# Kernel tuning notes

Measured on AMD Instinct MI355X. Metric: run time of the kernel, lower is better.

Reference implementation:

```python
import jax, jax.numpy as jnp
import numpy as np


def setup_inputs() -> dict:
    key = jax.random.key(0)
    ks = jax.random.split(key, 5)
    B, C, H, W = 4, 256, 64, 64
    Cq = C // 8
    x = jax.random.normal(ks[0], (B, C, H, W), dtype=jnp.float32)
    Wq = jax.random.normal(ks[1], (Cq, C), dtype=jnp.float32) * (1.0 / np.sqrt(C))
    Wk = jax.random.normal(ks[2], (Cq, C), dtype=jnp.float32) * (1.0 / np.sqrt(C))
    Wv = jax.random.normal(ks[3], (C, C), dtype=jnp.float32) * (1.0 / np.sqrt(C))
    bq = jnp.zeros((Cq,), dtype=jnp.float32)
    bk = jnp.zeros((Cq,), dtype=jnp.float32)
    bv = jnp.zeros((C,), dtype=jnp.float32)
    gamma = jnp.ones((1,), dtype=jnp.float32)
    return {"x": x, "Wq": Wq, "bq": bq, "Wk": Wk, "bk": bk, "Wv": Wv, "bv": bv, "gamma": gamma}


def reference(x, Wq, bq, Wk, bk, Wv, bv, gamma):
    B, C, H, W = x.shape
    N = H * W
    xf = x.reshape(B, C, N)                      # (B, C, N)
    # 1x1 convs == per-pixel linear projections over channels
    q = jnp.einsum('dc,bcn->bdn', Wq, xf) + bq[None, :, None]   # (B, C/8, N)
    k = jnp.einsum('dc,bcn->bdn', Wk, xf) + bk[None, :, None]   # (B, C/8, N)
    v = jnp.einsum('dc,bcn->bdn', Wv, xf) + bv[None, :, None]   # (B, C,   N)
    # attention: note original has NO 1/sqrt(d) scaling
    scores = jnp.einsum('bdn,bdm->bnm', q, k)     # (B, N, N)
    attn = jax.nn.softmax(scores, axis=-1)
    out = jnp.einsum('bnm,bdm->bnd', attn, v)     # (B, N, C)
    out = out.transpose(0, 2, 1).reshape(B, C, H, W)
    return gamma * out + x
```

## Files before the change

kernel.cpp:

```cpp
#include <hip/hip_runtime.h>

#define BATCH 4
#define CH    256
#define DQ    32
#define NPIX  4096
#define LOG2E 1.44269504088896340736f

typedef unsigned short u16;
typedef unsigned int   u32;
typedef __attribute__((ext_vector_type(8))) short short8;
typedef __attribute__((ext_vector_type(16))) float f32x16;

__device__ __align__(16) u16 g_wbf[10 * 2 * 8192];
__device__ float g_bias[10 * 32];

__device__ __forceinline__ float b2f(u32 u) {
  union { u32 i; float f; } v; v.i = (u & 0xffffu) << 16; return v.f;
}
__device__ __forceinline__ u16 f2b(float f) {
  union { float f; u32 i; } v; v.f = f;
  u32 x = v.i; x += 0x7fffu + ((x >> 16) & 1u);
  return (u16)(x >> 16);
}
__device__ __forceinline__ float fexp2(float x) {
#if __has_builtin(__builtin_amdgcn_exp2f)
  return __builtin_amdgcn_exp2f(x);
#else
  return __expf(x * 0.69314718055994530942f);
#endif
}

__device__ __forceinline__ void half_swap(u32 a0, u32 a1, u32 b0, u32 b1,
                                          int hl, uint4& o) {
#if __has_builtin(__builtin_amdgcn_permlane32_swap)
  const auto r0 = __builtin_amdgcn_permlane32_swap((int)a0, (int)b0, false, false);
  const auto r1 = __builtin_amdgcn_permlane32_swap((int)a1, (int)b1, false, false);
  o.x = (u32)r0[0]; o.y = (u32)r1[0]; o.z = (u32)r0[1]; o.w = (u32)r1[1];
#else
  const u32 s0 = hl ? a0 : b0;
  const u32 s1 = hl ? a1 : b1;
  const u32 r0 = (u32)__shfl_xor((int)s0, 32);
  const u32 r1 = (u32)__shfl_xor((int)s1, 32);
  o.x = hl ? r0 : a0; o.y = hl ? r1 : a1;
  o.z = hl ? b0 : r0; o.w = hl ? b1 : r1;
#endif
}

__global__ __launch_bounds__(256) void xprep(
    const float* __restrict__ x, u16* __restrict__ xt_hi, u16* __restrict__ xt_lo,
    const float* __restrict__ Wq, const float* __restrict__ bq,
    const float* __restrict__ Wk, const float* __restrict__ bk,
    const float* __restrict__ Wv, const float* __restrict__ bv)
{
  const int t = threadIdx.x;

  if (blockIdx.z == BATCH) {
    if (blockIdx.y != 0 || blockIdx.x >= 10) return;
    const int jt = blockIdx.x;
    const float* Wsrc; const float* bsrc; int jrow0; float scale = 1.f;
    if (jt == 0)      { Wsrc = Wq; bsrc = bq; jrow0 = 0; scale = LOG2E; }
    else if (jt == 1) { Wsrc = Wk; bsrc = bk; jrow0 = 0; }
    else              { Wsrc = Wv; bsrc = bv; jrow0 = (jt - 2) * 32; }
    u16* wdst = g_wbf + (size_t)jt * 16384;
    for (int i = 0; i < 32; ++i) {
      const int flat = i * 256 + t;
      const int j = flat >> 8, e = flat & 255;
      const float v = Wsrc[(size_t)(jrow0 + j) * CH + e] * scale;
      const u16 hi = f2b(v);
      const u16 lo = f2b(v - b2f(hi));
      const int idx = (((e >> 4) * 2 + ((e >> 3) & 1)) * 32 + j) * 8 + (e & 7);
      wdst[idx] = hi; wdst[8192 + idx] = lo;
    }
    if (t < 32) g_bias[jt * 32 + t] = bsrc[jrow0 + t] * scale;
    return;
  }

  const int nt = blockIdx.x, kb4 = blockIdx.y * 4, b = blockIdx.z;
  const int n0 = nt * 128, c0 = blockIdx.y * 64;
  __shared__ u32 xls[64][129];

  const int tn = t & 127, cp = t >> 7;
  for (int i = 0; i < 32; ++i) {
    const int c = cp + 2 * i;
    const float v = x[((size_t)b * CH + c0 + c) * NPIX + n0 + tn];
    const u16 h = f2b(v);
    const u16 l = f2b(v - b2f(h));
    xls[c][tn] = (u32)h | ((u32)l << 16);
  }
  __syncthreads();

  for (int rep = 0; rep < 4; ++rep) {
    const int id = t + 256 * rep;
    const int kkhl = id >> 7, n = id & 127;
    union { short8 s; uint4 u; } vh, vl;
    #pragma unroll
    for (int j = 0; j < 8; ++j) {
      const u32 p = xls[kkhl * 8 + j][n];
      vh.s[j] = (short)(p & 0xffffu);
      vl.s[j] = (short)(p >> 16);
    }
    const size_t o = ((((size_t)(b * 32 + nt) * 16 + kb4 + (kkhl >> 1)) * 2
                       + (kkhl & 1)) * 128 + n) * 8;
    *(uint4*)(xt_hi + o) = vh.u;
    *(uint4*)(xt_lo + o) = vl.u;
  }
}

__global__ __launch_bounds__(256, 4) void proj(
    const u16* __restrict__ xt_hi, const u16* __restrict__ xt_lo,
    u16* __restrict__ q_t, u16* __restrict__ k_t, u16* __restrict__ v_swz)
{
  const int L = blockIdx.x;
  const int xcd = L & 7, s = L >> 3;
  const int jt = s >> 4;
  const int pair = xcd * 16 + (s & 15);
  const int nt = pair >> 2, b = pair & 3;

  const int t = threadIdx.x;
  const int w = t >> 6, lane = t & 63, hl = lane >> 5, l31 = lane & 31;
  const int nb = w * 32 + l31, n = nt * 128 + nb;

  const u16* __restrict__ wb = g_wbf + (size_t)jt * 16384;
  const size_t xtile = (size_t)(b * 32 + nt) * 16 * 2 * 128 * 8;
  const u16* __restrict__ xh = xt_hi + xtile;
  const u16* __restrict__ xl = xt_lo + xtile;

  f32x16 acc1, acc2;
  #pragma unroll
  for (int r = 0; r < 16; ++r) { acc1[r] = 0.f; acc2[r] = 0.f; }

  #pragma unroll
  for (int kk = 0; kk < 16; ++kk) {
    const int aoff = ((kk * 2 + hl) * 32 + l31) * 8;
    const short8 wah = *(const short8*)(wb + aoff);
    const short8 wal = *(const short8*)(wb + 8192 + aoff);
    const int boff = ((kk * 2 + hl) * 128 + nb) * 8;
    const short8 xbh = *(const short8*)(xh + boff);
    const short8 xbl = *(const short8*)(xl + boff);
    acc1 = __builtin_amdgcn_mfma_f32_32x32x16_bf16(wah, xbh, acc1, 0, 0, 0);
    acc2 = __builtin_amdgcn_mfma_f32_32x32x16_bf16(wah, xbl, acc2, 0, 0, 0);
    acc2 = __builtin_amdgcn_mfma_f32_32x32x16_bf16(wal, xbh, acc2, 0, 0, 0);
  }

  f32x16 accv;
  #pragma unroll
  for (int r = 0; r < 16; ++r)
    accv[r] = acc1[r] + acc2[r]
            + g_bias[jt * 32 + (r & 3) + 8 * (r >> 2) + 4 * hl];

  if (jt <= 1) {
    u16* dst = (jt == 0) ? q_t : k_t;
    #pragma unroll
    for (int r2 = 0; r2 < 4; ++r2) {
      uint2 pk;
      pk.x = (u32)f2b(accv[4 * r2 + 0]) | ((u32)f2b(accv[4 * r2 + 1]) << 16);
      pk.y = (u32)f2b(accv[4 * r2 + 2]) | ((u32)f2b(accv[4 * r2 + 3]) << 16);
      *(uint2*)(dst + ((size_t)b * NPIX + n) * DQ + 4 * hl + 8 * r2) = pk;
    }
  } else {
    const int mc = nt * 4 + w;
    const int kc = (l31 >> 4) & 1, h3 = (l31 >> 3) & 1, j8 = l31 & 7;
    u16* dst = v_swz + (((((size_t)b * 128 + mc) * 8 + (jt - 2)) * 2 + kc) * 2 + h3) * 256 + j8;
    #pragma unroll
    for (int r = 0; r < 16; ++r) {
      const int c5 = (r & 3) + 8 * (r >> 2) + 4 * hl;
      dst[c5 * 8] = f2b(accv[r]);
    }
  }
}

__global__ __launch_bounds__(256, 2) void attn(
    const u16* __restrict__ q_t, const u16* __restrict__ k_t,
    const u16* __restrict__ v_swz, const float* __restrict__ x,
    const float* __restrict__ gamma, float* __restrict__ out)
{
  const int L = blockIdx.x;
  const int xcd = L & 7, slot = L >> 3;
  const int b = xcd >> 1;
  const int nt = slot * 2 + (xcd & 1);
  const int n0 = nt * 32;

  const int t = threadIdx.x;
  const int w = t >> 6, lane = t & 63, hl = lane >> 5, l31 = lane & 31;

  __shared__ float cbuf[8192];
  __shared__ float lbuf[4][64];

  short8 qf[2];
  #pragma unroll
  for (int kd = 0; kd < 2; ++kd)
    qf[kd] = *(const short8*)(q_t + ((size_t)b * NPIX + n0 + l31) * DQ + kd * 16 + hl * 8);

  f32x16 acc[8];
  #pragma unroll
  for (int ct = 0; ct < 8; ++ct)
    #pragma unroll
    for (int r = 0; r < 16; ++r) acc[ct][r] = 0.f;
  float lrun = 0.f;

  for (int cc = 0; cc < 32; ++cc) {
    const int mc = w * 32 + cc;

    const short8 kf0 = *(const short8*)(k_t + ((size_t)b * NPIX + mc * 32 + l31) * DQ + hl * 8);
    const short8 kf1 = *(const short8*)(k_t + ((size_t)b * NPIX + mc * 32 + l31) * DQ + 16 + hl * 8);
    f32x16 st;
    #pragma unroll
    for (int r = 0; r < 16; ++r) st[r] = 0.f;
    st = __builtin_amdgcn_mfma_f32_32x32x16_bf16(kf0, qf[0], st, 0, 0, 0);
    st = __builtin_amdgcn_mfma_f32_32x32x16_bf16(kf1, qf[1], st, 0, 0, 0);

    u32 pk[4][2];
    #pragma unroll
    for (int g = 0; g < 4; ++g) {
      const float e0 = fexp2(st[4 * g + 0]);
      const float e1 = fexp2(st[4 * g + 1]);
      const float e2 = fexp2(st[4 * g + 2]);
      const float e3 = fexp2(st[4 * g + 3]);
      lrun += (e0 + e1) + (e2 + e3);
      pk[g][0] = (u32)f2b(e0) | ((u32)f2b(e1) << 16);
      pk[g][1] = (u32)f2b(e2) | ((u32)f2b(e3) << 16);
    }

    const size_t vbase = ((size_t)b * 128 + mc) * 8192;
    #pragma unroll
    for (int kc = 0; kc < 2; ++kc) {
      union { uint4 u; short8 s; } bu;
      half_swap(pk[2 * kc][0], pk[2 * kc][1], pk[2 * kc + 1][0], pk[2 * kc + 1][1], hl, bu.u);
      #pragma unroll
      for (int ct = 0; ct < 8; ++ct) {
        const short8 av = *(const short8*)(v_swz + vbase + (size_t)(((ct * 2 + kc) * 2 + hl) * 256) + l31 * 8);
        acc[ct] = __builtin_amdgcn_mfma_f32_32x32x16_bf16(av, bu.s, acc[ct], 0, 0, 0);
      }
    }
  }

  lbuf[w][lane] = lrun;
  __syncthreads();
  for (int src = 1; src < 4; ++src) {
    if (w == src) {
      #pragma unroll
      for (int ct = 0; ct < 8; ++ct)
        #pragma unroll
        for (int r = 0; r < 16; ++r)
          cbuf[(ct * 16 + r) * 64 + lane] = acc[ct][r];
    }
    __syncthreads();
    if (w == 0) {
      #pragma unroll
      for (int ct = 0; ct < 8; ++ct)
        #pragma unroll
        for (int r = 0; r < 16; ++r)
          acc[ct][r] += cbuf[(ct * 16 + r) * 64 + lane];
    }
    __syncthreads();
  }

  if (w == 0) {
    float l = (lbuf[0][lane] + lbuf[1][lane]) + (lbuf[2][lane] + lbuf[3][lane]);
    l += __shfl_xor(l, 32);
    const float linv = 1.0f / l;
    const float g = gamma[0];
    #pragma unroll
    for (int ct = 0; ct < 8; ++ct)
      #pragma unroll
      for (int r = 0; r < 16; ++r) {
        const int c = ct * 32 + (r & 3) + 8 * (r >> 2) + 4 * hl;
        const size_t idx = ((size_t)b * CH + c) * NPIX + n0 + l31;
        out[idx] = g * acc[ct][r] * linv + x[idx];
      }
  }
}

extern "C" void kernel_launch(void* const* d_in, const int* in_sizes, int n_in,
                              void* d_out, int out_size, void* d_ws, size_t ws_size,
                              hipStream_t stream) {
  const float* x  = (const float*)d_in[0];
  const float* Wq = (const float*)d_in[1];
  const float* bq = (const float*)d_in[2];
  const float* Wk = (const float*)d_in[3];
  const float* bk = (const float*)d_in[4];
  const float* Wv = (const float*)d_in[5];
  const float* bv = (const float*)d_in[6];
  const float* gm = (const float*)d_in[7];
  float* out = (float*)d_out;

  const size_t qk_elems = (size_t)BATCH * NPIX * DQ;
  const size_t v_elems  = (size_t)BATCH * NPIX * CH;
  const size_t need = (2 * qk_elems + v_elems) * sizeof(u16);
  if (ws_size < need) return;

  u16* q_t   = (u16*)d_ws;
  u16* k_t   = q_t + qk_elems;
  u16* v_swz = k_t + qk_elems;

  u16* xt_hi = (u16*)d_out;
  u16* xt_lo = xt_hi + (size_t)BATCH * NPIX * CH;

  xprep<<<dim3(NPIX / 128, CH / 64, BATCH + 1), 256, 0, stream>>>(
      x, xt_hi, xt_lo, Wq, bq, Wk, bk, Wv, bv);
  proj<<<dim3(32 * 10 * BATCH), 256, 0, stream>>>(xt_hi, xt_lo, q_t, k_t, v_swz);
  attn<<<dim3((NPIX / 32) * BATCH), 256, 0, stream>>>(q_t, k_t, v_swz, x, gm, out);
}
```

Measured before the change: 160.3 us.

## Widen attention tile to 64 queries with 8 warps splitting keys and channels

The attention kernel now processes 64 query columns per block using 512 threads. Warps are split into 4 key groups by 2 channel halves, so each V fragment load feeds two MFMAs (one per 32-query subtile), halving V traffic per output. The cross-warp reduction now accumulates in shared memory with all threads doing a coalesced epilogue rather than warp 0 alone, and bf16 packing uses the hardware v_cvt_pk_bf16_f32 instruction. In exchange, shared memory doubles to 64KB plus accumulators per thread, which may cut occupancy, and the grid shrinks to 256 blocks.

```diff
diff --git a/kernel.cpp b/kernel.cpp
--- a/kernel.cpp
+++ b/kernel.cpp
@@ -28,6 +28,11 @@
 #else
   return __expf(x * 0.69314718055994530942f);
 #endif
+}
+__device__ __forceinline__ u32 cvtpk_bf16(float a, float b) {
+  u32 r;
+  asm("v_cvt_pk_bf16_f32 %0, %1, %2" : "=v"(r) : "v"(a), "v"(b));
+  return r;
 }
 
 __device__ __forceinline__ void half_swap(u32 a0, u32 a1, u32 b0, u32 b1,
@@ -169,7 +174,7 @@
   }
 }
 
-__global__ __launch_bounds__(256, 2) void attn(
+__global__ __launch_bounds__(512, 2) void attn(
     const u16* __restrict__ q_t, const u16* __restrict__ k_t,
     const u16* __restrict__ v_swz, const float* __restrict__ x,
     const float* __restrict__ gamma, float* __restrict__ out)
@@ -177,97 +182,115 @@
   const int L = blockIdx.x;
   const int xcd = L & 7, slot = L >> 3;
   const int b = xcd >> 1;
-  const int nt = slot * 2 + (xcd & 1);
-  const int n0 = nt * 32;
+  const int ng = slot * 2 + (xcd & 1);
+  const int n0 = ng * 64;
 
   const int t = threadIdx.x;
   const int w = t >> 6, lane = t & 63, hl = lane >> 5, l31 = lane & 31;
-
-  __shared__ float cbuf[8192];
-  __shared__ float lbuf[4][64];
-
-  short8 qf[2];
-  #pragma unroll
-  for (int kd = 0; kd < 2; ++kd)
-    qf[kd] = *(const short8*)(q_t + ((size_t)b * NPIX + n0 + l31) * DQ + kd * 16 + hl * 8);
-
-  f32x16 acc[8];
-  #pragma unroll
-  for (int ct = 0; ct < 8; ++ct)
-    #pragma unroll
-    for (int r = 0; r < 16; ++r) acc[ct][r] = 0.f;
-  float lrun = 0.f;
+  const int g = w >> 1, h = w & 1;
+
+  __shared__ float cbuf[16384];
+  __shared__ float lbuf[4][2][64];
+
+  short8 qf[2][2];
+  #pragma unroll
+  for (int jn = 0; jn < 2; ++jn)
+    #pragma unroll
+    for (int kd = 0; kd < 2; ++kd)
+      qf[jn][kd] = *(const short8*)(q_t + ((size_t)b * NPIX + n0 + jn * 32 + l31) * DQ + kd * 16 + hl * 8);
+
+  f32x16 acc[4][2];
+  #pragma unroll
+  for (int c = 0; c < 4; ++c)
+    #pragma unroll
+    for (int jn = 0; jn < 2; ++jn)
+      #pragma unroll
+      for (int r = 0; r < 16; ++r) acc[c][jn][r] = 0.f;
+  float lr[2] = {0.f, 0.f};
+
+  const u16* __restrict__ kb = k_t + (size_t)b * NPIX * DQ;
+  const u16* __restrict__ vb = v_swz + ((size_t)b * 128) * 8192
+                               + h * 4096 + hl * 256 + l31 * 8;
 
   for (int cc = 0; cc < 32; ++cc) {
-    const int mc = w * 32 + cc;
-
-    const short8 kf0 = *(const short8*)(k_t + ((size_t)b * NPIX + mc * 32 + l31) * DQ + hl * 8);
-    const short8 kf1 = *(const short8*)(k_t + ((size_t)b * NPIX + mc * 32 + l31) * DQ + 16 + hl * 8);
-    f32x16 st;
-    #pragma unroll
-    for (int r = 0; r < 16; ++r) st[r] = 0.f;
-    st = __builtin_amdgcn_mfma_f32_32x32x16_bf16(kf0, qf[0], st, 0, 0, 0);
-    st = __builtin_amdgcn_mfma_f32_32x32x16_bf16(kf1, qf[1], st, 0, 0, 0);
-
-    u32 pk[4][2];
-    #pragma unroll
-    for (int g = 0; g < 4; ++g) {
-      const float e0 = fexp2(st[4 * g + 0]);
-      const float e1 = fexp2(st[4 * g + 1]);
-      const float e2 = fexp2(st[4 * g + 2]);
-      const float e3 = fexp2(st[4 * g + 3]);
-      lrun += (e0 + e1) + (e2 + e3);
-      pk[g][0] = (u32)f2b(e0) | ((u32)f2b(e1) << 16);
-      pk[g][1] = (u32)f2b(e2) | ((u32)f2b(e3) << 16);
-    }
-
-    const size_t vbase = ((size_t)b * 128 + mc) * 8192;
-    #pragma unroll
-    for (int kc = 0; kc < 2; ++kc) {
-      union { uint4 u; short8 s; } bu;
-      half_swap(pk[2 * kc][0], pk[2 * kc][1], pk[2 * kc + 1][0], pk[2 * kc + 1][1], hl, bu.u);
-      #pragma unroll
-      for (int ct = 0; ct < 8; ++ct) {
-        const short8 av = *(const short8*)(v_swz + vbase + (size_t)(((ct * 2 + kc) * 2 + hl) * 256) + l31 * 8);
-        acc[ct] = __builtin_amdgcn_mfma_f32_32x32x16_bf16(av, bu.s, acc[ct], 0, 0, 0);
+    const int mc = g * 32 + cc;
+
+    const short8 kf0 = *(const short8*)(kb + (mc * 32 + l31) * DQ + hl * 8);
+    const short8 kf1 = *(const short8*)(kb + (mc * 32 + l31) * DQ + 16 + hl * 8);
+
+    u32 pk[2][4][2];
+    #pragma unroll
+    for (int jn = 0; jn < 2; ++jn) {
+      f32x16 st;
+      #pragma unroll
+      for (int r = 0; r < 16; ++r) st[r] = 0.f;
+      st = __builtin_amdgcn_mfma_f32_32x32x16_bf16(kf0, qf[jn][0], st, 0, 0, 0);
+      st = __builtin_amdgcn_mfma_f32_32x32x16_bf16(kf1, qf[jn][1], st, 0, 0, 0);
+      #pragma unroll
+      for (int g4 = 0; g4 < 4; ++g4) {
+        const float e0 = fexp2(st[4 * g4 + 0]);
+        const float e1 = fexp2(st[4 * g4 + 1]);
+        const float e2 = fexp2(st[4 * g4 + 2]);
+        const float e3 = fexp2(st[4 * g4 + 3]);
+        lr[jn] += (e0 + e1) + (e2 + e3);
+        pk[jn][g4][0] = cvtpk_bf16(e0, e1);
+        pk[jn][g4][1] = cvtpk_bf16(e2, e3);
       }
     }
-  }
-
-  lbuf[w][lane] = lrun;
+
+    union { uint4 u; short8 s; } bu[2][2];
+    #pragma unroll
+    for (int jn = 0; jn < 2; ++jn)
+      #pragma unroll
+      for (int kc = 0; kc < 2; ++kc)
+        half_swap(pk[jn][2 * kc][0], pk[jn][2 * kc][1],
+                  pk[jn][2 * kc + 1][0], pk[jn][2 * kc + 1][1], hl, bu[jn][kc].u);
+
+    const u16* __restrict__ vpt = vb + (size_t)mc * 8192;
+    #pragma unroll
+    for (int c = 0; c < 4; ++c)
+      #pragma unroll
+      for (int kc = 0; kc < 2; ++kc) {
+        const short8 av = *(const short8*)(vpt + c * 1024 + kc * 512);
+        acc[c][0] = __builtin_amdgcn_mfma_f32_32x32x16_bf16(av, bu[0][kc].s, acc[c][0], 0, 0, 0);
+        acc[c][1] = __builtin_amdgcn_mfma_f32_32x32x16_bf16(av, bu[1][kc].s, acc[c][1], 0, 0, 0);
+      }
+  }
+
+  if (h == 0) { lbuf[g][0][lane] = lr[0]; lbuf[g][1][lane] = lr[1]; }
+
+  for (int gs = 0; gs < 4; ++gs) {
+    __syncthreads();
+    if (g == gs) {
+      #pragma unroll
+      for (int c = 0; c < 4; ++c)
+        #pragma unroll
+        for (int jn = 0; jn < 2; ++jn)
+          #pragma unroll
+          for (int r = 0; r < 16; ++r) {
+            const int ch = (h * 4 + c) * 32 + (r & 3) + 8 * (r >> 2) + 4 * hl;
+            const int idx = (jn * 256 + ch) * 32 + l31;
+            if (gs == 0) cbuf[idx] = acc[c][jn][r];
+            else         cbuf[idx] += acc[c][jn][r];
+          }
+    }
+  }
   __syncthreads();
-  for (int src = 1; src < 4; ++src) {
-    if (w == src) {
-      #pragma unroll
-      for (int ct = 0; ct < 8; ++ct)
-        #pragma unroll
-        for (int r = 0; r < 16; ++r)
-          cbuf[(ct * 16 + r) * 64 + lane] = acc[ct][r];
-    }
-    __syncthreads();
-    if (w == 0) {
-      #pragma unroll
-      for (int ct = 0; ct < 8; ++ct)
-        #pragma unroll
-        for (int r = 0; r < 16; ++r)
-          acc[ct][r] += cbuf[(ct * 16 + r) * 64 + lane];
-    }
-    __syncthreads();
-  }
-
-  if (w == 0) {
-    float l = (lbuf[0][lane] + lbuf[1][lane]) + (lbuf[2][lane] + lbuf[3][lane]);
-    l += __shfl_xor(l, 32);
-    const float linv = 1.0f / l;
-    const float g = gamma[0];
-    #pragma unroll
-    for (int ct = 0; ct < 8; ++ct)
-      #pragma unroll
-      for (int r = 0; r < 16; ++r) {
-        const int c = ct * 32 + (r & 3) + 8 * (r >> 2) + 4 * hl;
-        const size_t idx = ((size_t)b * CH + c) * NPIX + n0 + l31;
-        out[idx] = g * acc[ct][r] * linv + x[idx];
-      }
+
+  const int col = t & 63, chg = t >> 6;
+  const int jn = col >> 5, c31 = col & 31;
+  float l = 0.f;
+  #pragma unroll
+  for (int gg = 0; gg < 4; ++gg)
+    l += lbuf[gg][jn][c31] + lbuf[gg][jn][c31 + 32];
+  const float linv = 1.0f / l;
+  const float gmv = gamma[0];
+  #pragma unroll
+  for (int i = 0; i < 32; ++i) {
+    const int ch = chg * 32 + i;
+    const float cb = cbuf[(jn * 256 + ch) * 32 + c31];
+    const size_t oidx = ((size_t)b * CH + ch) * NPIX + n0 + col;
+    out[oidx] = gmv * cb * linv + x[oidx];
   }
 }
 
@@ -299,5 +322,5 @@
   xprep<<<dim3(NPIX / 128, CH / 64, BATCH + 1), 256, 0, stream>>>(
       x, xt_hi, xt_lo, Wq, bq, Wk, bk, Wv, bv);
   proj<<<dim3(32 * 10 * BATCH), 256, 0, stream>>>(xt_hi, xt_lo, q_t, k_t, v_swz);
-  attn<<<dim3((NPIX / 32) * BATCH), 256, 0, stream>>>(q_t, k_t, v_swz, x, gm, out);
-}
+  attn<<<dim3((NPIX / 64) * BATCH), 512, 0, stream>>>(q_t, k_t, v_swz, x, gm, out);
+}
```

Result: slower. 173.7 us (+8.3%).

## Double-buffer V fragments in registers and software-pipeline QK scores in attention loop

Applied to the files above, without the earlier changes.

Restructures the attention main loop into a two-stage software pipeline. V tiles for the next key chunk are loaded into a second register buffer while the current chunk's exp and PV MFMAs run, and the next QK score MFMA is issued before the PV products. It also replaces the manual bf16 rounding with the packed v_cvt_pk_bf16_f32 instruction and relaxes launch bounds to one block per SM so the larger register footprint fits. This trades occupancy for latency hiding through explicit prefetch.

```diff
diff --git a/kernel.cpp b/kernel.cpp
--- a/kernel.cpp
+++ b/kernel.cpp
@@ -28,6 +28,11 @@
 #else
   return __expf(x * 0.69314718055994530942f);
 #endif
+}
+__device__ __forceinline__ u32 cvtpk_bf16(float a, float b) {
+  u32 r;
+  asm("v_cvt_pk_bf16_f32 %0, %1, %2" : "=v"(r) : "v"(a), "v"(b));
+  return r;
 }
 
 __device__ __forceinline__ void half_swap(u32 a0, u32 a1, u32 b0, u32 b1,
@@ -169,7 +174,7 @@
   }
 }
 
-__global__ __launch_bounds__(256, 2) void attn(
+__global__ __launch_bounds__(256, 1) void attn(
     const u16* __restrict__ q_t, const u16* __restrict__ k_t,
     const u16* __restrict__ v_swz, const float* __restrict__ x,
     const float* __restrict__ gamma, float* __restrict__ out)
@@ -198,18 +203,41 @@
     for (int r = 0; r < 16; ++r) acc[ct][r] = 0.f;
   float lrun = 0.f;
 
-  for (int cc = 0; cc < 32; ++cc) {
-    const int mc = w * 32 + cc;
-
-    const short8 kf0 = *(const short8*)(k_t + ((size_t)b * NPIX + mc * 32 + l31) * DQ + hl * 8);
-    const short8 kf1 = *(const short8*)(k_t + ((size_t)b * NPIX + mc * 32 + l31) * DQ + 16 + hl * 8);
-    f32x16 st;
-    #pragma unroll
-    for (int r = 0; r < 16; ++r) st[r] = 0.f;
-    st = __builtin_amdgcn_mfma_f32_32x32x16_bf16(kf0, qf[0], st, 0, 0, 0);
-    st = __builtin_amdgcn_mfma_f32_32x32x16_bf16(kf1, qf[1], st, 0, 0, 0);
-
-    u32 pk[4][2];
+  const u16* __restrict__ kb = k_t + (size_t)b * NPIX * DQ;
+  const u16* __restrict__ vp = v_swz + ((size_t)b * 128) * 8192
+                               + hl * 256 + l31 * 8;
+
+  short8 va[16], vb[16];
+
+  auto vload = [&](short8* A, int mcx) {
+    const u16* vt = vp + (size_t)mcx * 8192;
+    #pragma unroll
+    for (int kc = 0; kc < 2; ++kc)
+      #pragma unroll
+      for (int ct = 0; ct < 8; ++ct)
+        A[kc * 8 + ct] = *(const short8*)(vt + (ct * 2 + kc) * 512);
+  };
+  auto sstep = [&](int mcx) {
+    const short8 kf0 = *(const short8*)(kb + (mcx * 32 + l31) * DQ + hl * 8);
+    const short8 kf1 = *(const short8*)(kb + (mcx * 32 + l31) * DQ + 16 + hl * 8);
+    f32x16 s;
+    #pragma unroll
+    for (int r = 0; r < 16; ++r) s[r] = 0.f;
+    s = __builtin_amdgcn_mfma_f32_32x32x16_bf16(kf0, qf[0], s, 0, 0, 0);
+    s = __builtin_amdgcn_mfma_f32_32x32x16_bf16(kf1, qf[1], s, 0, 0, 0);
+    return s;
+  };
+
+  vload(va, w * 32);
+  f32x16 st = sstep(w * 32);
+
+  for (int cc2 = 0; cc2 < 16; ++cc2) {
+    const int mcA = w * 32 + 2 * cc2;
+    const int mcB = mcA + 1;
+    const int mcN = (2 * cc2 + 1 < 31) ? mcB + 1 : mcB;
+
+    vload(vb, mcB);
+    u32 pkA[4][2];
     #pragma unroll
     for (int g = 0; g < 4; ++g) {
       const float e0 = fexp2(st[4 * g + 0]);
@@ -217,20 +245,39 @@
       const float e2 = fexp2(st[4 * g + 2]);
       const float e3 = fexp2(st[4 * g + 3]);
       lrun += (e0 + e1) + (e2 + e3);
-      pk[g][0] = (u32)f2b(e0) | ((u32)f2b(e1) << 16);
-      pk[g][1] = (u32)f2b(e2) | ((u32)f2b(e3) << 16);
-    }
-
-    const size_t vbase = ((size_t)b * 128 + mc) * 8192;
+      pkA[g][0] = cvtpk_bf16(e0, e1);
+      pkA[g][1] = cvtpk_bf16(e2, e3);
+    }
+    st = sstep(mcB);
     #pragma unroll
     for (int kc = 0; kc < 2; ++kc) {
       union { uint4 u; short8 s; } bu;
-      half_swap(pk[2 * kc][0], pk[2 * kc][1], pk[2 * kc + 1][0], pk[2 * kc + 1][1], hl, bu.u);
-      #pragma unroll
-      for (int ct = 0; ct < 8; ++ct) {
-        const short8 av = *(const short8*)(v_swz + vbase + (size_t)(((ct * 2 + kc) * 2 + hl) * 256) + l31 * 8);
-        acc[ct] = __builtin_amdgcn_mfma_f32_32x32x16_bf16(av, bu.s, acc[ct], 0, 0, 0);
-      }
+      half_swap(pkA[2 * kc][0], pkA[2 * kc][1], pkA[2 * kc + 1][0], pkA[2 * kc + 1][1], hl, bu.u);
+      #pragma unroll
+      for (int ct = 0; ct < 8; ++ct)
+        acc[ct] = __builtin_amdgcn_mfma_f32_32x32x16_bf16(va[kc * 8 + ct], bu.s, acc[ct], 0, 0, 0);
+    }
+
+    vload(va, mcN);
+    u32 pkB[4][2];
+    #pragma unroll
+    for (int g = 0; g < 4; ++g) {
+      const float e0 = fexp2(st[4 * g + 0]);
+      const float e1 = fexp2(st[4 * g + 1]);
+      const float e2 = fexp2(st[4 * g + 2]);
+      const float e3 = fexp2(st[4 * g + 3]);
+      lrun += (e0 + e1) + (e2 + e3);
+      pkB[g][0] = cvtpk_bf16(e0, e1);
+      pkB[g][1] = cvtpk_bf16(e2, e3);
+    }
+    st = sstep(mcN);
+    #pragma unroll
+    for (int kc = 0; kc < 2; ++kc) {
+      union { uint4 u; short8 s; } bu;
+      half_swap(pkB[2 * kc][0], pkB[2 * kc][1], pkB[2 * kc + 1][0], pkB[2 * kc + 1][1], hl, bu.u);
+      #pragma unroll
+      for (int ct = 0; ct < 8; ++ct)
+        acc[ct] = __builtin_amdgcn_mfma_f32_32x32x16_bf16(vb[kc * 8 + ct], bu.s, acc[ct], 0, 0, 0);
     }
   }
 
```

After: 172.2 us. 1.07x slower.
